# Optimization experiments

Hardware: AMD Instinct MI355X
Metric: run time of the kernel (lower is better)

Reference implementation:

```python
import jax, jax.numpy as jnp
import numpy as np


def setup_inputs() -> dict:
    key = jax.random.key(0)
    k1, k2 = jax.random.split(key)
    B, C, H, W = 8, 21, 512, 512
    inp = jax.random.normal(k1, (B, C, H, W), dtype=jnp.float32)
    target = jax.random.randint(k2, (B, H, W), 0, C, dtype=jnp.int64)
    return {"input": inp, "target": target}


def reference(input, target):
    # input: (B, C, H, W) logits; target: (B, H, W) int labels in [0, C)
    B, C, H, W = input.shape
    N = H * W
    logits = input.reshape(B, C, N)                      # (B, C, N)
    tgt = target.reshape(B, N)                           # (B, N)
    tgt_f = tgt.astype(logits.dtype)

    probs = jax.nn.softmax(logits, axis=1)               # (B, C, N)
    # foreground mask per class: (B, C, N)
    fg = (tgt[:, None, :] == jnp.arange(C)[None, :, None]).astype(logits.dtype)
    errors = jnp.abs(fg - probs)                         # (B, C, N)

    # descending sort along N, vectorized over all (B, C) rows
    perm = jnp.argsort(-errors, axis=2)                  # (B, C, N)
    errors_sorted = jnp.take_along_axis(errors, perm, axis=2)
    # faithful to kornia: gather the raw float labels (not the binary mask)
    tgt_bc = jnp.broadcast_to(tgt_f[:, None, :], (B, C, N))
    target_sorted = jnp.take_along_axis(tgt_bc, perm, axis=2)  # (B, C, N)

    tsum = jnp.sum(target_sorted, axis=2, keepdims=True)       # (B, C, 1)
    intersection = tsum - jnp.cumsum(target_sorted, axis=2)
    union = tsum + jnp.cumsum(1.0 - target_sorted, axis=2)
    gradient = 1.0 - intersection / union                      # (B, C, N)
    # in-place diff along last axis: g[..., 1:] -= g[..., :-1]
    gradient = jnp.concatenate(
        [gradient[..., :1], gradient[..., 1:] - gradient[..., :-1]], axis=-1
    )

    # per-class loss = mean over batch of sum over pixels; final = mean over classes
    loss_bc = jnp.sum(jax.nn.relu(errors_sorted) * gradient, axis=2)  # (B, C)
    return jnp.mean(loss_bc)
```

## Files before the change

kernel.cpp:

```cpp
#include <hip/hip_runtime.h>


#define NB     8
#define NC     21
#define NPIX   262144
#define NROWS  (NB * NC)
#define NBINS  768
#define CHUNKS 64
#define CHUNK  (NPIX / CHUNKS)

__global__ __launch_bounds__(512, 4) void k_fused(
    const float* __restrict__ x,
    const int* __restrict__ tgt,
    unsigned long long* __restrict__ ghist) {
  __shared__ unsigned hist[NC * NBINS];
  int tid = threadIdx.x;
  for (int i = tid; i < NC * NBINS; i += 512) hist[i] = 0;
  __syncthreads();

  int b     = blockIdx.x >> 6;
  int chunk = blockIdx.x & 63;
  const float* xb = x + (size_t)b * NC * NPIX + (size_t)chunk * CHUNK;
  const int*   tb = tgt + (size_t)b * NPIX + (size_t)chunk * CHUNK;

  #pragma unroll
  for (int g = 0; g < 4; ++g) {
    int n2 = (g * 512 + tid) * 2;

    float v[NC][2];
    float m[2] = {-3.4e38f, -3.4e38f};
    #pragma unroll
    for (int c = 0; c < NC; ++c) {
      float2 t = *(const float2*)(xb + (size_t)c * NPIX + n2);
      v[c][0] = t.x; v[c][1] = t.y;
      m[0] = fmaxf(m[0], t.x); m[1] = fmaxf(m[1], t.y);
    }
    float Z[2] = {0.f, 0.f};
    #pragma unroll
    for (int c = 0; c < NC; ++c) {
      #pragma unroll
      for (int j = 0; j < 2; ++j) {
        v[c][j] = __expf(v[c][j] - m[j]);
        Z[j] += v[c][j];
      }
    }
    float iZ[2];
    #pragma unroll
    for (int j = 0; j < 2; ++j) iZ[j] = 1.0f / Z[j];

    int2 tv = *(const int2*)(tb + n2);
    int tl[2] = {tv.x, tv.y};

    #pragma unroll
    for (int c = 0; c < NC; ++c) {
      unsigned* hr = hist + c * NBINS;
      #pragma unroll
      for (int j = 0; j < 2; ++j) {
        float p = v[c][j] * iZ[j];
        float e = fabsf(((c == tl[j]) ? 1.0f : 0.0f) - p);
        unsigned fb   = __float_as_uint(e);
        int      fexp = (int)(fb >> 23) - 127;
        unsigned key;
        if (fexp < -12) key = 0u;
        else {
          key = (((unsigned)(fexp + 12)) << 6) | ((fb >> 17) & 63u);
          if (key > NBINS - 1) key = NBINS - 1;
        }
        atomicAdd(hr + key, (1u << 18) | (unsigned)tl[j]);
      }
    }
  }
  __syncthreads();

  unsigned long long* gh = ghist + (size_t)b * NC * NBINS;
  for (int i = tid; i < NC * NBINS; i += 512) {
    unsigned v = hist[i];
    if (v)
      atomicAdd(gh + i,
                ((unsigned long long)(v >> 18) << 32) | (unsigned long long)(v & 0x3FFFFu));
  }
}

__device__ inline unsigned long long shfl_up_u64(unsigned long long v, int off) {
  unsigned lo = (unsigned)v, hi = (unsigned)(v >> 32);
  lo = (unsigned)__shfl_up((int)lo, off, 64);
  hi = (unsigned)__shfl_up((int)hi, off, 64);
  return ((unsigned long long)hi << 32) | lo;
}
__device__ inline unsigned long long shfl_down_u64(unsigned long long v, int off) {
  unsigned lo = (unsigned)v, hi = (unsigned)(v >> 32);
  lo = (unsigned)__shfl_down((int)lo, off, 64);
  hi = (unsigned)__shfl_down((int)hi, off, 64);
  return ((unsigned long long)hi << 32) | lo;
}

__global__ __launch_bounds__(768) void k_scan(
    const unsigned long long* __restrict__ ghist,
    float* __restrict__ out) {
  int row  = blockIdx.x;
  int tid  = threadIdx.x;
  int lane = tid & 63;
  int wave = tid >> 6;

  __shared__ unsigned long long hist0[NBINS];
  __shared__ unsigned long long wtot[12];
  __shared__ double wred[12];
  __shared__ double sT;

  hist0[tid] = ghist[(size_t)row * NBINS + tid];
  __syncthreads();

  unsigned long long tot = hist0[tid];
  #pragma unroll
  for (int off = 32; off > 0; off >>= 1) tot += shfl_down_u64(tot, off);
  if (lane == 0) wtot[wave] = tot;
  __syncthreads();
  if (tid == 0) {
    unsigned long long g = 0;
    #pragma unroll
    for (int w = 0; w < 12; ++w) g += wtot[w];
    sT = (double)(unsigned)(g & 0xffffffffULL);
  }
  __syncthreads();
  double T = sT;
  __syncthreads();

  int bin = (NBINS - 1) - tid;
  unsigned long long v = hist0[bin];

  unsigned long long s = v;
  #pragma unroll
  for (int off = 1; off < 64; off <<= 1) {
    unsigned long long u = shfl_up_u64(s, off);
    if (lane >= off) s += u;
  }
  if (lane == 63) wtot[wave] = s;
  __syncthreads();

  unsigned long long woff = 0;
  for (int w = 0; w < wave; ++w) woff += wtot[w];
  unsigned long long excl = s - v + woff;

  double acc = 0.0;
  unsigned n = (unsigned)(v >> 32);
  if (n) {
    unsigned sl = (unsigned)(v & 0xffffffffu);
    unsigned cb = (unsigned)(excl >> 32);
    unsigned sb = (unsigned)(excl & 0xffffffffu);
    double Sb = (double)sb + (double)sl;
    double gb = 1.0 - (T - Sb) / (T + (double)(cb + n) - Sb);
    double ga = (cb == 0) ? 0.0
                          : 1.0 - (T - (double)sb) / (T + (double)cb - (double)sb);
    unsigned key = (unsigned)bin;
    unsigned ex  = key >> 6, mant = key & 63u;
    float e = ldexpf(1.0f + ((float)mant + 0.5f) * 0.015625f, (int)ex - 12);
    acc = (double)e * (gb - ga);
  }

  #pragma unroll
  for (int off = 32; off > 0; off >>= 1) acc += __shfl_down(acc, off, 64);
  if (lane == 0) wred[wave] = acc;
  __syncthreads();
  if (tid == 0) {
    double ssum = 0.0;
    #pragma unroll
    for (int w = 0; w < 12; ++w) ssum += wred[w];
    atomicAdd(out, (float)(ssum * (1.0 / (double)NROWS)));
  }
}

extern "C" void kernel_launch(void* const* d_in, const int* in_sizes, int n_in,
                              void* d_out, int out_size, void* d_ws, size_t ws_size,
                              hipStream_t stream) {
  const float* x  = (const float*)d_in[0];
  const int* tgt  = (const int*)d_in[1];
  float* out      = (float*)d_out;
  unsigned long long* ghist = (unsigned long long*)d_ws;

  hipMemsetAsync(d_out, 0, sizeof(float), stream);
  hipMemsetAsync(ghist, 0, (size_t)NROWS * NBINS * sizeof(unsigned long long), stream);
  k_fused<<<NB * CHUNKS, 512, 0, stream>>>(x, tgt, ghist);
  k_scan<<<NROWS, NBINS, 0, stream>>>(ghist, out);
}
```

Baseline: 281.2 us.

## Restructure histogram kernel with fp16 LDS staging and grouped class histograms

The fused kernel now processes one pixel per thread in 1024-thread blocks over 1024-pixel chunks. It stages the logits as fp16 in shared memory and computes the softmax normalizer as a log-sum-exp without max subtraction. Class histograms are built in three groups of 7 classes, so the shared histogram is much smaller, which is meant to raise occupancy and parallelism. In exchange the grid is four times larger, so there are many more global 64-bit atomic flushes and extra barriers. The fp16 staging and the missing max shift also add precision and overflow risk.

```diff
diff --git a/kernel.cpp b/kernel.cpp
--- a/kernel.cpp
+++ b/kernel.cpp
@@ -6,78 +6,64 @@
 #define NPIX   262144
 #define NROWS  (NB * NC)
 #define NBINS  768
-#define CHUNKS 64
-#define CHUNK  (NPIX / CHUNKS)
+#define CHUNK  1024
+#define CPB    (NPIX / CHUNK)
+#define G      7
 
-__global__ __launch_bounds__(512, 4) void k_fused(
+__global__ __launch_bounds__(1024, 8) void k_fused(
     const float* __restrict__ x,
     const int* __restrict__ tgt,
     unsigned long long* __restrict__ ghist) {
-  __shared__ unsigned hist[NC * NBINS];
-  int tid = threadIdx.x;
-  for (int i = tid; i < NC * NBINS; i += 512) hist[i] = 0;
-  __syncthreads();
+  __shared__ _Float16 stage[NC][CHUNK];
+  __shared__ unsigned hist[G * NBINS];
+  int tid   = threadIdx.x;
+  int b     = blockIdx.x >> 8;
+  int chunk = blockIdx.x & (CPB - 1);
+  const float* xb = x + (size_t)b * NC * NPIX + (size_t)chunk * CHUNK;
 
-  int b     = blockIdx.x >> 6;
-  int chunk = blockIdx.x & 63;
-  const float* xb = x + (size_t)b * NC * NPIX + (size_t)chunk * CHUNK;
-  const int*   tb = tgt + (size_t)b * NPIX + (size_t)chunk * CHUNK;
+  for (int i = tid; i < G * NBINS; i += 1024) hist[i] = 0;
 
+  float Z = 0.f;
   #pragma unroll
-  for (int g = 0; g < 4; ++g) {
-    int n2 = (g * 512 + tid) * 2;
-
-    float v[NC][2];
-    float m[2] = {-3.4e38f, -3.4e38f};
-    #pragma unroll
-    for (int c = 0; c < NC; ++c) {
-      float2 t = *(const float2*)(xb + (size_t)c * NPIX + n2);
-      v[c][0] = t.x; v[c][1] = t.y;
-      m[0] = fmaxf(m[0], t.x); m[1] = fmaxf(m[1], t.y);
-    }
-    float Z[2] = {0.f, 0.f};
-    #pragma unroll
-    for (int c = 0; c < NC; ++c) {
-      #pragma unroll
-      for (int j = 0; j < 2; ++j) {
-        v[c][j] = __expf(v[c][j] - m[j]);
-        Z[j] += v[c][j];
-      }
-    }
-    float iZ[2];
-    #pragma unroll
-    for (int j = 0; j < 2; ++j) iZ[j] = 1.0f / Z[j];
-
-    int2 tv = *(const int2*)(tb + n2);
-    int tl[2] = {tv.x, tv.y};
-
-    #pragma unroll
-    for (int c = 0; c < NC; ++c) {
-      unsigned* hr = hist + c * NBINS;
-      #pragma unroll
-      for (int j = 0; j < 2; ++j) {
-        float p = v[c][j] * iZ[j];
-        float e = fabsf(((c == tl[j]) ? 1.0f : 0.0f) - p);
-        unsigned fb   = __float_as_uint(e);
-        int      fexp = (int)(fb >> 23) - 127;
-        unsigned key;
-        if (fexp < -12) key = 0u;
-        else {
-          key = (((unsigned)(fexp + 12)) << 6) | ((fb >> 17) & 63u);
-          if (key > NBINS - 1) key = NBINS - 1;
-        }
-        atomicAdd(hr + key, (1u << 18) | (unsigned)tl[j]);
-      }
-    }
+  for (int c = 0; c < NC; ++c) {
+    float t = xb[(size_t)c * NPIX + tid];
+    Z += __expf(t);
+    stage[c][tid] = (_Float16)t;
   }
+  float L = __logf(Z);
+  unsigned lab = (unsigned)tgt[(size_t)b * NPIX + (size_t)chunk * CHUNK + tid];
   __syncthreads();
 
   unsigned long long* gh = ghist + (size_t)b * NC * NBINS;
-  for (int i = tid; i < NC * NBINS; i += 512) {
-    unsigned v = hist[i];
-    if (v)
-      atomicAdd(gh + i,
-                ((unsigned long long)(v >> 18) << 32) | (unsigned long long)(v & 0x3FFFFu));
+  for (int grp = 0; grp < 3; ++grp) {
+    #pragma unroll
+    for (int j = 0; j < G; ++j) {
+      int c = grp * G + j;
+      float xv = (float)stage[c][tid];
+      float p  = __expf(xv - L);
+      float e  = fabsf(((c == (int)lab) ? 1.0f : 0.0f) - p);
+      unsigned fb = __float_as_uint(e);
+      int      fx = (int)(fb >> 23) - 127;
+      unsigned k;
+      if (fx < -12) k = 0u;
+      else {
+        k = (((unsigned)(fx + 12)) << 6) | ((fb >> 17) & 63u);
+        if (k > NBINS - 1) k = NBINS - 1;
+      }
+      atomicAdd(hist + j * NBINS + k, (1u << 18) | lab);
+    }
+    __syncthreads();
+    for (int i = tid; i < G * NBINS; i += 1024) {
+      unsigned v = hist[i];
+      if (v) {
+        int j = i / NBINS, bin = i - j * NBINS;
+        atomicAdd(gh + (size_t)(grp * G + j) * NBINS + bin,
+                  ((unsigned long long)(v >> 18) << 32) |
+                  (unsigned long long)(v & 0x3FFFFu));
+        hist[i] = 0;
+      }
+    }
+    __syncthreads();
   }
 }
 
@@ -179,6 +165,6 @@
 
   hipMemsetAsync(d_out, 0, sizeof(float), stream);
   hipMemsetAsync(ghist, 0, (size_t)NROWS * NBINS * sizeof(unsigned long long), stream);
-  k_fused<<<NB * CHUNKS, 512, 0, stream>>>(x, tgt, ghist);
+  k_fused<<<NB * CPB, 1024, 0, stream>>>(x, tgt, ghist);
   k_scan<<<NROWS, NBINS, 0, stream>>>(ghist, out);
 }
```

Result: slower. 355.3 us (+26.3%).
